# Kernel tuning notes

Hardware: AMD Instinct MI355X
Metric: run time of the kernel (lower is better)

The kernel has to match this reference:

```python
import jax, jax.numpy as jnp
import numpy as np

N, M, D = 8192, 8192, 64

def setup_inputs() -> dict:
    key = jax.random.key(0)
    ka, kb = jax.random.split(key)
    a = jax.random.normal(ka, (N, D), dtype=jnp.float32)
    b = jax.random.normal(kb, (M, D), dtype=jnp.float32)
    return {"a": a, "b": b}

def reference(a, b):
    # pairwise cosine similarity: (a @ b.T) / (|a| outer |b|)
    numer = jnp.einsum('nd,md->nm', a, b)          # [N, M]
    anorms = jnp.linalg.norm(a, axis=1)            # [N]
    bnorms = jnp.linalg.norm(b, axis=1)            # [M]
    return numer / (anorms[:, None] * bnorms[None, :])
```

## Files before the change

kernel.cpp:

```cpp
#include <hip/hip_runtime.h>
#include <hip/hip_bf16.h>
#include <cstdint>
#include <cstddef>

typedef short short8 __attribute__((ext_vector_type(8)));
typedef float f32x4 __attribute__((ext_vector_type(4)));

constexpr int Nrows = 8192;
constexpr int Mrows = 8192;
constexpr int Dim   = 64;

__global__ __launch_bounds__(256) void cos_norm_scale(
    const float* __restrict__ a, const float* __restrict__ b,
    short* __restrict__ as_, short* __restrict__ bs_) {
  int gid = blockIdx.x * 256 + threadIdx.x;
  int row = gid >> 4;
  int sub = gid & 15;
  const float* src = a;
  short* dst = as_;
  if (row >= Nrows) { src = b; dst = bs_; row -= Nrows; }

  float4 v = reinterpret_cast<const float4*>(src + (size_t)row * Dim)[sub];
  float ss = v.x * v.x + v.y * v.y + v.z * v.z + v.w * v.w;
  ss += __shfl_xor(ss, 1);
  ss += __shfl_xor(ss, 2);
  ss += __shfl_xor(ss, 4);
  ss += __shfl_xor(ss, 8);
  float scale = rsqrtf(ss);

  float sv[4] = {v.x * scale, v.y * scale, v.z * scale, v.w * scale};
  short4 o;
  short* op = reinterpret_cast<short*>(&o);
#pragma unroll
  for (int i = 0; i < 4; ++i) {
    uint32_t u = __float_as_uint(sv[i]);
    u += 0x7fffu + ((u >> 16) & 1u);
    op[i] = (short)(u >> 16);
  }
  reinterpret_cast<short4*>(dst + (size_t)row * Dim)[sub] = o;
}

__global__ __launch_bounds__(256) void cos_gemm(
    const short* __restrict__ A, const short* __restrict__ B,
    float* __restrict__ C) {
  int tile = blockIdx.x;
  int tm = tile >> 6;
  int tn = tile & 63;
  int wid  = threadIdx.x >> 6;
  int lane = threadIdx.x & 63;
  int wr = wid >> 1, wc = wid & 1;

  int R0 = tm * 128 + wr * 64;
  int C0 = tn * 128 + wc * 64;

  int lrow = lane & 15;
  int lk8  = (lane >> 4) * 8;

  f32x4 acc[4][4] = {};

#pragma unroll
  for (int s = 0; s < 2; ++s) {
    short8 af[4], bf[4];
#pragma unroll
    for (int i = 0; i < 4; ++i)
      af[i] = *reinterpret_cast<const short8*>(
          A + (size_t)(R0 + i * 16 + lrow) * Dim + s * 32 + lk8);
#pragma unroll
    for (int j = 0; j < 4; ++j)
      bf[j] = *reinterpret_cast<const short8*>(
          B + (size_t)(C0 + j * 16 + lrow) * Dim + s * 32 + lk8);
#pragma unroll
    for (int i = 0; i < 4; ++i)
#pragma unroll
      for (int j = 0; j < 4; ++j)
        acc[i][j] = __builtin_amdgcn_mfma_f32_16x16x32_bf16(
            af[i], bf[j], acc[i][j], 0, 0, 0);
  }

  int crow = (lane >> 4) * 4;
  int ccol = lane & 15;
#pragma unroll
  for (int i = 0; i < 4; ++i) {
#pragma unroll
    for (int j = 0; j < 4; ++j) {
      float* p = C + (size_t)(R0 + i * 16 + crow) * Mrows + (C0 + j * 16 + ccol);
#pragma unroll
      for (int r = 0; r < 4; ++r)
        p[(size_t)r * Mrows] = acc[i][j][r];
    }
  }
}

extern "C" void kernel_launch(void* const* d_in, const int* in_sizes, int n_in,
                              void* d_out, int out_size, void* d_ws, size_t ws_size,
                              hipStream_t stream) {
  const float* a = (const float*)d_in[0];
  const float* b = (const float*)d_in[1];
  float* out = (float*)d_out;

  short* as_ = (short*)d_ws;
  short* bs_ = as_ + (size_t)Nrows * Dim;

  cos_norm_scale<<<1024, 256, 0, stream>>>(a, b, as_, bs_);

  cos_gemm<<<4096, 256, 0, stream>>>(as_, bs_, out);
}
```

Before: 61.49 us.

## Fuse row normalization into GEMM and stage output through LDS for vector stores

Removes the separate normalize-and-convert kernel. Each GEMM block now loads fp32 rows directly, computes the row norms with cross-lane shuffles, scales the rows and converts them to bf16 in registers before the MFMAs. The output tile is staged through shared memory so each lane writes contiguous float4 values with nontemporal stores, replacing scattered scalar stores. In exchange, every block recomputes norms for its 128 rows and 128 columns, reads fp32 inputs (twice the bytes of bf16), and uses 68 KB of LDS, which may limit occupancy.

Result: slower. 75.25 us (+22.4%).

```diff
diff --git a/kernel.cpp b/kernel.cpp
--- a/kernel.cpp
+++ b/kernel.cpp
@@ -6,43 +6,21 @@
 typedef short short8 __attribute__((ext_vector_type(8)));
 typedef float f32x4 __attribute__((ext_vector_type(4)));
 
-constexpr int Nrows = 8192;
-constexpr int Mrows = 8192;
-constexpr int Dim   = 64;
+constexpr int NR = 8192;
+constexpr int MR = 8192;
+constexpr int D  = 64;
 
-__global__ __launch_bounds__(256) void cos_norm_scale(
-    const float* __restrict__ a, const float* __restrict__ b,
-    short* __restrict__ as_, short* __restrict__ bs_) {
-  int gid = blockIdx.x * 256 + threadIdx.x;
-  int row = gid >> 4;
-  int sub = gid & 15;
-  const float* src = a;
-  short* dst = as_;
-  if (row >= Nrows) { src = b; dst = bs_; row -= Nrows; }
-
-  float4 v = reinterpret_cast<const float4*>(src + (size_t)row * Dim)[sub];
-  float ss = v.x * v.x + v.y * v.y + v.z * v.z + v.w * v.w;
-  ss += __shfl_xor(ss, 1);
-  ss += __shfl_xor(ss, 2);
-  ss += __shfl_xor(ss, 4);
-  ss += __shfl_xor(ss, 8);
-  float scale = rsqrtf(ss);
-
-  float sv[4] = {v.x * scale, v.y * scale, v.z * scale, v.w * scale};
-  short4 o;
-  short* op = reinterpret_cast<short*>(&o);
-#pragma unroll
-  for (int i = 0; i < 4; ++i) {
-    uint32_t u = __float_as_uint(sv[i]);
-    u += 0x7fffu + ((u >> 16) & 1u);
-    op[i] = (short)(u >> 16);
-  }
-  reinterpret_cast<short4*>(dst + (size_t)row * Dim)[sub] = o;
+__device__ inline short f2bf(float f) {
+  uint32_t u = __float_as_uint(f);
+  u += 0x7fffu + ((u >> 16) & 1u);
+  return (short)(u >> 16);
 }
 
-__global__ __launch_bounds__(256) void cos_gemm(
-    const short* __restrict__ A, const short* __restrict__ B,
+__global__ __launch_bounds__(256, 2) void cos_fused(
+    const float* __restrict__ A, const float* __restrict__ B,
     float* __restrict__ C) {
+  __shared__ float lds[4][64][68];
+
   int tile = blockIdx.x;
   int tm = tile >> 6;
   int tn = tile & 63;
@@ -56,38 +34,78 @@
   int lrow = lane & 15;
   int lk8  = (lane >> 4) * 8;
 
-  f32x4 acc[4][4] = {};
+  short8 af[4][2], bf[4][2];
 
 #pragma unroll
-  for (int s = 0; s < 2; ++s) {
-    short8 af[4], bf[4];
+  for (int i = 0; i < 4; ++i) {
+    const float* p = A + (size_t)(R0 + i * 16 + lrow) * D + lk8;
+    float v[16];
+    *reinterpret_cast<float4*>(v)      = *reinterpret_cast<const float4*>(p);
+    *reinterpret_cast<float4*>(v + 4)  = *reinterpret_cast<const float4*>(p + 4);
+    *reinterpret_cast<float4*>(v + 8)  = *reinterpret_cast<const float4*>(p + 32);
+    *reinterpret_cast<float4*>(v + 12) = *reinterpret_cast<const float4*>(p + 36);
+    float ss = 0.f;
 #pragma unroll
-    for (int i = 0; i < 4; ++i)
-      af[i] = *reinterpret_cast<const short8*>(
-          A + (size_t)(R0 + i * 16 + lrow) * Dim + s * 32 + lk8);
+    for (int e = 0; e < 16; ++e) ss += v[e] * v[e];
+    ss += __shfl_xor(ss, 16);
+    ss += __shfl_xor(ss, 32);
+    float sc = rsqrtf(ss);
+    short t[16];
 #pragma unroll
-    for (int j = 0; j < 4; ++j)
-      bf[j] = *reinterpret_cast<const short8*>(
-          B + (size_t)(C0 + j * 16 + lrow) * Dim + s * 32 + lk8);
+    for (int e = 0; e < 16; ++e) t[e] = f2bf(v[e] * sc);
+    af[i][0] = *reinterpret_cast<short8*>(t);
+    af[i][1] = *reinterpret_cast<short8*>(t + 8);
+  }
+
+#pragma unroll
+  for (int j = 0; j < 4; ++j) {
+    const float* p = B + (size_t)(C0 + j * 16 + lrow) * D + lk8;
+    float v[16];
+    *reinterpret_cast<float4*>(v)      = *reinterpret_cast<const float4*>(p);
+    *reinterpret_cast<float4*>(v + 4)  = *reinterpret_cast<const float4*>(p + 4);
+    *reinterpret_cast<float4*>(v + 8)  = *reinterpret_cast<const float4*>(p + 32);
+    *reinterpret_cast<float4*>(v + 12) = *reinterpret_cast<const float4*>(p + 36);
+    float ss = 0.f;
+#pragma unroll
+    for (int e = 0; e < 16; ++e) ss += v[e] * v[e];
+    ss += __shfl_xor(ss, 16);
+    ss += __shfl_xor(ss, 32);
+    float sc = rsqrtf(ss);
+    short t[16];
+#pragma unroll
+    for (int e = 0; e < 16; ++e) t[e] = f2bf(v[e] * sc);
+    bf[j][0] = *reinterpret_cast<short8*>(t);
+    bf[j][1] = *reinterpret_cast<short8*>(t + 8);
+  }
+
+  f32x4 acc[4][4] = {};
+#pragma unroll
+  for (int s = 0; s < 2; ++s)
 #pragma unroll
     for (int i = 0; i < 4; ++i)
 #pragma unroll
       for (int j = 0; j < 4; ++j)
         acc[i][j] = __builtin_amdgcn_mfma_f32_16x16x32_bf16(
-            af[i], bf[j], acc[i][j], 0, 0, 0);
-  }
+            af[i][s], bf[j][s], acc[i][j], 0, 0, 0);
 
   int crow = (lane >> 4) * 4;
   int ccol = lane & 15;
 #pragma unroll
-  for (int i = 0; i < 4; ++i) {
+  for (int i = 0; i < 4; ++i)
 #pragma unroll
-    for (int j = 0; j < 4; ++j) {
-      float* p = C + (size_t)(R0 + i * 16 + crow) * Mrows + (C0 + j * 16 + ccol);
+    for (int j = 0; j < 4; ++j)
 #pragma unroll
       for (int r = 0; r < 4; ++r)
-        p[(size_t)r * Mrows] = acc[i][j][r];
-    }
+        lds[wid][i * 16 + crow + r][j * 16 + ccol] = acc[i][j][r];
+
+#pragma unroll
+  for (int it = 0; it < 16; ++it) {
+    int row = it * 4 + (lane >> 4);
+    int col = (lane & 15) * 4;
+    f32x4 o = *reinterpret_cast<const f32x4*>(&lds[wid][row][col]);
+    f32x4* dst = reinterpret_cast<f32x4*>(
+        C + (size_t)(R0 + row) * MR + (C0 + col));
+    __builtin_nontemporal_store(o, dst);
   }
 }
 
@@ -98,10 +116,5 @@
   const float* b = (const float*)d_in[1];
   float* out = (float*)d_out;
 
-  short* as_ = (short*)d_ws;
-  short* bs_ = as_ + (size_t)Nrows * Dim;
-
-  cos_norm_scale<<<1024, 256, 0, stream>>>(a, b, as_, bs_);
-
-  cos_gemm<<<4096, 256, 0, stream>>>(as_, bs_, out);
+  cos_fused<<<4096, 256, 0, stream>>>(a, b, out);
 }
```

## Retile GEMM to 16x1024 strips per block with one A fragment per wave

Applied to the files above, without the earlier changes.

The GEMM block tiling changes from 128x128 tiles (2x2 waves, each 64x64) to 16-row by 1024-column strips, where each wave computes 16x256 using a single A fragment and sixteen B fragments. A block now covers whole contiguous row segments, so output stores are aimed at more contiguous writes and each block writes full lines of C. In exchange, B is reloaded far more often from global/L2, since each B fragment is reused by only 16 rows instead of 64, and per-wave arithmetic intensity drops.

New measurement: 87.55 us. +42.4%, slower.

```diff
diff --git a/kernel.cpp b/kernel.cpp
--- a/kernel.cpp
+++ b/kernel.cpp
@@ -43,50 +43,41 @@
 __global__ __launch_bounds__(256) void cos_gemm(
     const short* __restrict__ A, const short* __restrict__ B,
     float* __restrict__ C) {
-  int tile = blockIdx.x;
-  int tm = tile >> 6;
-  int tn = tile & 63;
+  int bid = blockIdx.x;
+  int tm = bid >> 3;
+  int tn = bid & 7;
   int wid  = threadIdx.x >> 6;
   int lane = threadIdx.x & 63;
-  int wr = wid >> 1, wc = wid & 1;
 
-  int R0 = tm * 128 + wr * 64;
-  int C0 = tn * 128 + wc * 64;
+  int R0 = tm * 16;
+  int C0 = tn * 1024 + wid * 256;
 
   int lrow = lane & 15;
   int lk8  = (lane >> 4) * 8;
 
-  f32x4 acc[4][4] = {};
+  f32x4 acc[16] = {};
 
 #pragma unroll
   for (int s = 0; s < 2; ++s) {
-    short8 af[4], bf[4];
+    short8 af = *reinterpret_cast<const short8*>(
+        A + (size_t)(R0 + lrow) * Dim + s * 32 + lk8);
+    short8 bf[16];
 #pragma unroll
-    for (int i = 0; i < 4; ++i)
-      af[i] = *reinterpret_cast<const short8*>(
-          A + (size_t)(R0 + i * 16 + lrow) * Dim + s * 32 + lk8);
-#pragma unroll
-    for (int j = 0; j < 4; ++j)
+    for (int j = 0; j < 16; ++j)
       bf[j] = *reinterpret_cast<const short8*>(
           B + (size_t)(C0 + j * 16 + lrow) * Dim + s * 32 + lk8);
 #pragma unroll
-    for (int i = 0; i < 4; ++i)
-#pragma unroll
-      for (int j = 0; j < 4; ++j)
-        acc[i][j] = __builtin_amdgcn_mfma_f32_16x16x32_bf16(
-            af[i], bf[j], acc[i][j], 0, 0, 0);
+    for (int j = 0; j < 16; ++j)
+      acc[j] = __builtin_amdgcn_mfma_f32_16x16x32_bf16(af, bf[j], acc[j], 0, 0, 0);
   }
 
   int crow = (lane >> 4) * 4;
   int ccol = lane & 15;
 #pragma unroll
-  for (int i = 0; i < 4; ++i) {
+  for (int r = 0; r < 4; ++r) {
 #pragma unroll
-    for (int j = 0; j < 4; ++j) {
-      float* p = C + (size_t)(R0 + i * 16 + crow) * Mrows + (C0 + j * 16 + ccol);
-#pragma unroll
-      for (int r = 0; r < 4; ++r)
-        p[(size_t)r * Mrows] = acc[i][j][r];
+    for (int j = 0; j < 16; ++j) {
+      C[(size_t)(R0 + crow + r) * Mrows + (C0 + j * 16 + ccol)] = acc[j][r];
     }
   }
 }
@@ -102,6 +93,5 @@
   short* bs_ = as_ + (size_t)Nrows * Dim;
 
   cos_norm_scale<<<1024, 256, 0, stream>>>(a, b, as_, bs_);
-
   cos_gemm<<<4096, 256, 0, stream>>>(as_, bs_, out);
 }
```
